# Performance work log

Hardware: AMD Instinct MI355X
Metric: run time of the kernel (lower is better)

Reference implementation:

```python
import jax, jax.numpy as jnp
import numpy as np

DIM = 512
A_HEADS = 8
C_HEADS = 4
DH = 64
EPS = 1e-5


def layer_norm(x, g, b):
    mu = jnp.mean(x, axis=-1, keepdims=True)
    var = jnp.var(x, axis=-1, keepdims=True)
    return (x - mu) * jax.lax.rsqrt(var + EPS) * g + b


def setup_inputs() -> dict:
    key = jax.random.key(0)
    ks = jax.random.split(key, 8)
    inner_a = A_HEADS * DH  # 512
    inner_c = C_HEADS * DH  # 256
    s = 0.02
    return {
        "x": jax.random.normal(ks[0], (4, 192, DIM), dtype=jnp.float32),
        # Attention branch params
        "ln1_g": jnp.ones((DIM,), jnp.float32),
        "ln1_b": jnp.zeros((DIM,), jnp.float32),
        "Wqkv": jax.random.normal(ks[1], (DIM, 3 * inner_a), jnp.float32) * s,
        "Wo": jax.random.normal(ks[2], (inner_a, DIM), jnp.float32) * s,
        "bo": jnp.zeros((DIM,), jnp.float32),
        # Trittention branch params
        "ln2_g": jnp.ones((DIM,), jnp.float32),
        "ln2_b": jnp.zeros((DIM,), jnp.float32),
        "Wabcde": jax.random.normal(ks[3], (DIM, 5 * inner_c), jnp.float32) * s,
        "babcde": jnp.zeros((5 * inner_c,), jnp.float32),
        "Wp": jax.random.normal(ks[4], (inner_c, DIM), jnp.float32) * s,
        "bp": jnp.zeros((DIM,), jnp.float32),
    }


def _attention(x, ln_g, ln_b, Wqkv, Wo, bo):
    B, T, _ = x.shape
    xn = layer_norm(x, ln_g, ln_b)
    qkv = xn @ Wqkv  # [B,T,3*H*D]
    q, k, v = jnp.split(qkv, 3, axis=-1)
    def heads(t):
        return t.reshape(B, T, A_HEADS, DH).transpose(0, 2, 1, 3)  # [B,H,T,D]
    q, k, v = heads(q), heads(k), heads(v)
    scale = DH ** -0.5
    dots = jnp.einsum('bhqd,bhkd->bhqk', q, k) * scale
    attn = jax.nn.softmax(dots, axis=-1)
    out = jnp.einsum('bhqk,bhkd->bhqd', attn, v)
    out = out.transpose(0, 2, 1, 3).reshape(B, T, A_HEADS * DH)
    return out @ Wo + bo


def _trittention(x, ln_g, ln_b, Wabcde, babcde, Wp, bp):
    B, T, _ = x.shape
    xn = layer_norm(x, ln_g, ln_b)
    proj = xn @ Wabcde + babcde  # [B,T,5*H*D]
    a, b_, c, d_, e = jnp.split(proj, 5, axis=-1)
    def heads(t):
        return t.reshape(B, T, C_HEADS, DH)  # [B,T,H,D]
    a, b_, c, d_, e = heads(a), heads(b_), heads(c), heads(d_), heads(e)
    # cubic score: [B,H,S,T,Q]
    score = jnp.einsum('bshd,bthd,bqhd->bhstq', a, b_, c) / DH
    # softmax over joint (s,t) for each query q
    score = score.transpose(0, 1, 4, 2, 3).reshape(B, C_HEADS, T, T * T)
    attn = jax.nn.softmax(score, axis=-1).reshape(B, C_HEADS, T, T, T)
    z = (jnp.einsum('bhqst,bshd->bhqd', attn, d_)
         + jnp.einsum('bhqst,bthd->bhqd', attn, e))
    z = z.transpose(0, 2, 1, 3).reshape(B, T, C_HEADS * DH)
    return z @ Wp + bp


def reference(x, ln1_g, ln1_b, Wqkv, Wo, bo, ln2_g, ln2_b, Wabcde, babcde, Wp, bp):
    return (_attention(x, ln1_g, ln1_b, Wqkv, Wo, bo)
            + _trittention(x, ln2_g, ln2_b, Wabcde, babcde, Wp, bp))
```

## Files before the change

kernel.cpp:

```cpp
#include <hip/hip_runtime.h>
#include <cstdint>


#define B_   4
#define T_   192
#define DIM_ 512
#define AH   8
#define CH   4

typedef unsigned short u16;
typedef unsigned int   u32;
typedef __attribute__((ext_vector_type(8))) short short8;
typedef __attribute__((ext_vector_type(4))) float floatx4;
typedef __attribute__((ext_vector_type(4))) int intx4;
typedef __attribute__((ext_vector_type(2))) float f32x2;
typedef __attribute__((ext_vector_type(8))) _Float16 half8;
typedef __attribute__((ext_vector_type(2))) _Float16 half2v;
typedef __attribute__((ext_vector_type(2))) __fp16 fp16x2;

union Frag  { intx4 i; short8 s; };
union FragH { intx4 i; half8 h; };

__device__ __forceinline__ floatx4 mfma16(Frag a, Frag b, floatx4 c) {
    return __builtin_amdgcn_mfma_f32_16x16x32_bf16(a.s, b.s, c, 0, 0, 0);
}
__device__ __forceinline__ floatx4 mfma16h(FragH a, FragH b, floatx4 c) {
    return __builtin_amdgcn_mfma_f32_16x16x32_f16(a.h, b.h, c, 0, 0, 0);
}

__device__ __forceinline__ float fexp2(float x) {
    return __builtin_amdgcn_exp2f(x);
}

__device__ __forceinline__ float wave_reduce_sum(float v) {
#pragma unroll
    for (int off = 32; off >= 1; off >>= 1)
        v += __shfl_xor(v, off, 64);
    return v;
}

__device__ __forceinline__ u32 pack_rne(float x, float y) {
    u32 ux = __float_as_uint(x);
    u32 uy = __float_as_uint(y);
    ux += 0x7fffu + ((ux >> 16) & 1u);
    uy += 0x7fffu + ((uy >> 16) & 1u);
    return (ux >> 16) | (uy & 0xffff0000u);
}
__device__ __forceinline__ u16 bf16_rne(float x) {
    u32 u = __float_as_uint(x);
    u += 0x7fffu + ((u >> 16) & 1u);
    return (u16)(u >> 16);
}
__device__ __forceinline__ float bf16f(u16 h) { return __uint_as_float(((u32)h) << 16); }

__device__ __forceinline__ u32 pack_f16(float x, float y) {
    union { fp16x2 h; u32 u; } cv;
    cv.h = __builtin_amdgcn_cvt_pkrtz(x, y);
    return cv.u;
}
__device__ __forceinline__ u32 mul_h2(u32 a, u32 b) {
    union { u32 u; half2v h; } ua, ub, uw;
    ua.u = a; ub.u = b;
    uw.h = ua.h * ub.h;
    return uw.u;
}

__device__ __forceinline__ Frag ld_frag8(const u16* p) {
    Frag f;
    uint2 a = *(const uint2*)p;
    uint2 b = *(const uint2*)(p + 4);
    f.i = (intx4){ (int)a.x, (int)a.y, (int)b.x, (int)b.y };
    return f;
}

#define LOG2E 1.44269504088896f

__global__ __launch_bounds__(256) void prep_kernel(
    const float* __restrict__ x,
    const float* __restrict__ g1, const float* __restrict__ b1,
    const float* __restrict__ g2, const float* __restrict__ b2,
    u16* __restrict__ x1h, u16* __restrict__ x2h,
    const float* __restrict__ Wqkv, u16* __restrict__ wqh,
    const float* __restrict__ Wab,  u16* __restrict__ wah,
    const float* __restrict__ Wo,   const float* __restrict__ Wp,
    u16* __restrict__ wofh)
{
    __shared__ union { float t[64][65]; float red[4][2]; } u;
    const int tid = threadIdx.x;
    if (blockIdx.x < 768) {
        int row = blockIdx.x;
        const float2 v = ((const float2*)(x + (size_t)row * DIM_))[tid];
        float s  = v.x + v.y;
        float s2 = v.x * v.x + v.y * v.y;
        s  = wave_reduce_sum(s);
        s2 = wave_reduce_sum(s2);
        int w = tid >> 6;
        if ((tid & 63) == 0) { u.red[w][0] = s; u.red[w][1] = s2; }
        __syncthreads();
        float ts  = u.red[0][0] + u.red[1][0] + u.red[2][0] + u.red[3][0];
        float ts2 = u.red[0][1] + u.red[1][1] + u.red[2][1] + u.red[3][1];
        float mean = ts * (1.0f / DIM_);
        float var  = ts2 * (1.0f / DIM_) - mean * mean;
        float rstd = rsqrtf(var + 1e-5f);
        int c0 = tid * 2;
        float n0 = (v.x - mean) * rstd;
        float n1 = (v.y - mean) * rstd;
        float a0 = n0 * g1[c0] + b1[c0], a1 = n1 * g1[c0 + 1] + b1[c0 + 1];
        float c2 = n0 * g2[c0] + b2[c0], c3 = n1 * g2[c0 + 1] + b2[c0 + 1];
        size_t o = (size_t)row * 256 + tid;
        ((u32*)x1h)[o] = pack_rne(a0, a1);
        ((u32*)x2h)[o] = pack_rne(c2, c3);
        return;
    }
    int id = blockIdx.x - 768;
    const float* W; u16 *H; int K, N, Kout, kofs, tile;
    if (id < 192)      { W = Wqkv; H = wqh;  K = 512; N = 1536; Kout = 512; kofs = 0;   tile = id;       }
    else if (id < 352) { W = Wab;  H = wah;  K = 512; N = 1280; Kout = 512; kofs = 0;   tile = id - 192; }
    else if (id < 416) { W = Wo;   H = wofh; K = 512; N = 512;  Kout = 768; kofs = 0;   tile = id - 352; }
    else               { W = Wp;   H = wofh; K = 256; N = 512;  Kout = 768; kofs = 512; tile = id - 416; }
    int nx = N >> 6;
    int n0 = (tile % nx) * 64, k0 = (tile / nx) * 64;
    int rr = tid >> 4, c4 = (tid & 15) << 2;
#pragma unroll
    for (int p = 0; p < 4; ++p) {
        int row = rr + p * 16;
        float4 v = *(const float4*)(W + (size_t)(k0 + row) * N + n0 + c4);
        u.t[row][c4 + 0] = v.x; u.t[row][c4 + 1] = v.y;
        u.t[row][c4 + 2] = v.z; u.t[row][c4 + 3] = v.w;
    }
    __syncthreads();
#pragma unroll
    for (int p = 0; p < 4; ++p) {
        int n = rr + p * 16;
        u16 hi[4];
#pragma unroll
        for (int c = 0; c < 4; ++c)
            hi[c] = bf16_rne(u.t[c4 + c][n]);
        size_t o = (size_t)(n0 + n) * Kout + kofs + k0 + c4;
        *(uint2*)&H[o] = make_uint2((u32)hi[0] | ((u32)hi[1] << 16), (u32)hi[2] | ((u32)hi[3] << 16));
    }
}

__global__ __launch_bounds__(256) void gemm_dual(
    const u16* __restrict__ x1h, const u16* __restrict__ wqh,
    const u16* __restrict__ x2h, const u16* __restrict__ wah,
    const float* __restrict__ babcde,
    float* __restrict__ qkv, float* __restrict__ proj)
{
    __shared__ u16 As[64][68];
    __shared__ u16 Bs[64][68];
    const int tid = threadIdx.x;
    const int nb = blockIdx.x;
    const u16 *Ah, *BTh; const float* bias; float* C; int N, bn;
    if (nb < 24) { Ah = x1h; BTh = wqh; bias = nullptr; C = qkv;  N = 1536; bn = nb * 64; }
    else         { Ah = x2h; BTh = wah; bias = babcde; C = proj; N = 1280; bn = (nb - 24) * 64; }
    const int K = 512;
    const int bm = blockIdx.y * 64;
    const int lane = tid & 63, wave = tid >> 6;
    const int m16 = lane & 15, quad = lane >> 4;
    const int wm = (wave >> 1) * 32, wn = (wave & 1) * 32;
    const int r = tid >> 2, c16 = (tid & 3) * 16;

    floatx4 acc[2][2];
#pragma unroll
    for (int i = 0; i < 2; ++i)
#pragma unroll
        for (int j = 0; j < 2; ++j) acc[i][j] = (floatx4){0.f, 0.f, 0.f, 0.f};

    for (int k0 = 0; k0 < K; k0 += 64) {
        __syncthreads();
        {
            const u16* pa = Ah + (size_t)(bm + r) * K + k0 + c16;
            uint4 v0 = *(const uint4*)pa, v1 = *(const uint4*)(pa + 8);
            *(uint2*)&As[r][c16 + 0]  = make_uint2(v0.x, v0.y);
            *(uint2*)&As[r][c16 + 4]  = make_uint2(v0.z, v0.w);
            *(uint2*)&As[r][c16 + 8]  = make_uint2(v1.x, v1.y);
            *(uint2*)&As[r][c16 + 12] = make_uint2(v1.z, v1.w);
        }
        {
            const u16* pb = BTh + (size_t)(bn + r) * K + k0 + c16;
            uint4 v0 = *(const uint4*)pb, v1 = *(const uint4*)(pb + 8);
            *(uint2*)&Bs[r][c16 + 0]  = make_uint2(v0.x, v0.y);
            *(uint2*)&Bs[r][c16 + 4]  = make_uint2(v0.z, v0.w);
            *(uint2*)&Bs[r][c16 + 8]  = make_uint2(v1.x, v1.y);
            *(uint2*)&Bs[r][c16 + 12] = make_uint2(v1.z, v1.w);
        }
        __syncthreads();
#pragma unroll
        for (int ks = 0; ks < 2; ++ks) {
            const int ko = ks * 32 + quad * 8;
            Frag a0 = ld_frag8(&As[wm + m16][ko]);
            Frag a1 = ld_frag8(&As[wm + 16 + m16][ko]);
            Frag b0 = ld_frag8(&Bs[wn + m16][ko]);
            Frag b1 = ld_frag8(&Bs[wn + 16 + m16][ko]);
            acc[0][0] = mfma16(a0, b0, acc[0][0]);
            acc[0][1] = mfma16(a0, b1, acc[0][1]);
            acc[1][0] = mfma16(a1, b0, acc[1][0]);
            acc[1][1] = mfma16(a1, b1, acc[1][1]);
        }
    }
#pragma unroll
    for (int i = 0; i < 2; ++i)
#pragma unroll
        for (int rr = 0; rr < 4; ++rr) {
            int m = bm + wm + i * 16 + quad * 4 + rr;
#pragma unroll
            for (int j = 0; j < 2; ++j) {
                int n = bn + wn + j * 16 + m16;
                float v = acc[i][j][rr];
                if (bias) v += bias[n];
                C[(size_t)m * N + n] = v;
            }
        }
}

__global__ __launch_bounds__(256) void gemm_epilogue(
    const u16* __restrict__ aoh, const u16* __restrict__ zh,
    const u16* __restrict__ BTh,
    const float* __restrict__ bo, const float* __restrict__ bp,
    float* __restrict__ C)
{
    __shared__ u16 As[32][68];
    __shared__ u16 Bs[64][68];
    const int tid = threadIdx.x;
    const int bm = blockIdx.y * 32, bn = blockIdx.x * 64;
    const int lane = tid & 63, wave = tid >> 6;
    const int m16 = lane & 15, quad = lane >> 4;
    const int wm = (wave >> 1) * 16, wn = (wave & 1) * 32;
    const int ra = tid >> 3, c8 = (tid & 7) * 8;
    const int rb = tid >> 2, c16 = (tid & 3) * 16;
    const int N = 512, K = 768;

    floatx4 acc[2];
    acc[0] = (floatx4){0.f, 0.f, 0.f, 0.f};
    acc[1] = (floatx4){0.f, 0.f, 0.f, 0.f};

    for (int k0 = 0; k0 < K; k0 += 64) {
        __syncthreads();
        {
            const u16* pah = (k0 < 512)
                ? aoh + (size_t)(bm + ra) * 512 + k0 + c8
                : zh  + (size_t)(bm + ra) * 256 + (k0 - 512) + c8;
            uint4 v = *(const uint4*)pah;
            *(uint2*)&As[ra][c8 + 0] = make_uint2(v.x, v.y);
            *(uint2*)&As[ra][c8 + 4] = make_uint2(v.z, v.w);
        }
        {
            const u16* pb = BTh + (size_t)(bn + rb) * K + k0 + c16;
            uint4 v0 = *(const uint4*)pb, v1 = *(const uint4*)(pb + 8);
            *(uint2*)&Bs[rb][c16 + 0]  = make_uint2(v0.x, v0.y);
            *(uint2*)&Bs[rb][c16 + 4]  = make_uint2(v0.z, v0.w);
            *(uint2*)&Bs[rb][c16 + 8]  = make_uint2(v1.x, v1.y);
            *(uint2*)&Bs[rb][c16 + 12] = make_uint2(v1.z, v1.w);
        }
        __syncthreads();
#pragma unroll
        for (int ks = 0; ks < 2; ++ks) {
            const int ko = ks * 32 + quad * 8;
            Frag ah = ld_frag8(&As[wm + m16][ko]);
            Frag b0 = ld_frag8(&Bs[wn + m16][ko]);
            Frag b1 = ld_frag8(&Bs[wn + 16 + m16][ko]);
            acc[0] = mfma16(ah, b0, acc[0]);
            acc[1] = mfma16(ah, b1, acc[1]);
        }
    }
#pragma unroll
    for (int rr = 0; rr < 4; ++rr) {
        int m = bm + wm + quad * 4 + rr;
#pragma unroll
        for (int j = 0; j < 2; ++j) {
            int n = bn + wn + j * 16 + m16;
            C[(size_t)m * N + n] = acc[j][rr] + bo[n] + bp[n];
        }
    }
}

__global__ __launch_bounds__(256) void attn_mfma(
    const float* __restrict__ qkv, u16* __restrict__ aoh, float* __restrict__ zero_base)
{
    __shared__ union { u16 Ks[192][68]; u16 P[32][196]; } KP;
    __shared__ union { u16 Vt[64][196]; struct { float m[2][16][68]; float r[2][16]; } mg; } VU;
    const int qt = blockIdx.x, h = blockIdx.y, b = blockIdx.z;
    const int tid = threadIdx.x;
    {
        float4* z4 = (float4*)zero_base;
        const float4 z = make_float4(0.f, 0.f, 0.f, 0.f);
        int gid = ((b * AH + h) * 6 + qt) * 256 + tid;
        for (int i = gid; i < 294912; i += 49152) z4[i] = z;
    }
    const int lane = tid & 63, wave = tid >> 6;
    const int m16 = lane & 15, quad = lane >> 4;
    const int qg = wave & 1;
    const int kh = wave >> 1;
    const size_t base = (size_t)(b * T_) * 1536 + h * 64;

    for (int i = tid; i < 192 * 16; i += 256) {
        int row = i >> 4, c4 = (i & 15) << 2;
        float4 kv = *(const float4*)(qkv + base + (size_t)row * 1536 + 512 + c4);
        *(uint2*)&KP.Ks[row][c4] = make_uint2(pack_rne(kv.x, kv.y), pack_rne(kv.z, kv.w));
        float4 vv = *(const float4*)(qkv + base + (size_t)row * 1536 + 1024 + c4);
        VU.Vt[c4 + 0][row] = bf16_rne(vv.x);
        VU.Vt[c4 + 1][row] = bf16_rne(vv.y);
        VU.Vt[c4 + 2][row] = bf16_rne(vv.z);
        VU.Vt[c4 + 3][row] = bf16_rne(vv.w);
    }

    Frag qf0, qf1;
    {
        const float s = 0.125f * LOG2E;
        const float* qp = qkv + base + (size_t)(qt * 32 + qg * 16 + m16) * 1536 + quad * 8;
        float4 u0 = *(const float4*)qp;
        float4 u1 = *(const float4*)(qp + 4);
        float4 u2 = *(const float4*)(qp + 32);
        float4 u3 = *(const float4*)(qp + 36);
        qf0.i = (intx4){ (int)pack_rne(u0.x * s, u0.y * s), (int)pack_rne(u0.z * s, u0.w * s),
                         (int)pack_rne(u1.x * s, u1.y * s), (int)pack_rne(u1.z * s, u1.w * s) };
        qf1.i = (intx4){ (int)pack_rne(u2.x * s, u2.y * s), (int)pack_rne(u2.z * s, u2.w * s),
                         (int)pack_rne(u3.x * s, u3.y * s), (int)pack_rne(u3.z * s, u3.w * s) };
    }
    __syncthreads();

    float ev[6][4];
    float rsum[4] = {0.f, 0.f, 0.f, 0.f};
#pragma unroll
    for (int tt = 0; tt < 6; ++tt) {
        const int krow = kh * 96 + tt * 16 + m16;
        Frag kb0 = ld_frag8(&KP.Ks[krow][quad * 8]);
        Frag kb1 = ld_frag8(&KP.Ks[krow][32 + quad * 8]);
        floatx4 accs = (floatx4){0.f, 0.f, 0.f, 0.f};
        accs = mfma16(qf0, kb0, accs);
        accs = mfma16(qf1, kb1, accs);
#pragma unroll
        for (int rr = 0; rr < 4; ++rr) {
            float e = fexp2(accs[rr]);
            ev[tt][rr] = e;
            rsum[rr] += e;
        }
    }
#pragma unroll
    for (int rr = 0; rr < 4; ++rr) {
        float v = rsum[rr];
        v += __shfl_xor(v, 1, 64);
        v += __shfl_xor(v, 2, 64);
        v += __shfl_xor(v, 4, 64);
        v += __shfl_xor(v, 8, 64);
        rsum[rr] = v;
    }

    __syncthreads();
#pragma unroll
    for (int tt = 0; tt < 6; ++tt)
#pragma unroll
        for (int rr = 0; rr < 4; ++rr)
            KP.P[qg * 16 + quad * 4 + rr][kh * 96 + tt * 16 + m16] = bf16_rne(ev[tt][rr]);

    floatx4 acco[4];
#pragma unroll
    for (int dt = 0; dt < 4; ++dt) acco[dt] = (floatx4){0.f, 0.f, 0.f, 0.f};
#pragma unroll
    for (int ts = 0; ts < 3; ++ts) {
        Frag pf = ld_frag8(&KP.P[qg * 16 + m16][kh * 96 + ts * 32 + quad * 8]);
#pragma unroll
        for (int dt = 0; dt < 4; ++dt) {
            Frag vf = ld_frag8(&VU.Vt[dt * 16 + m16][kh * 96 + ts * 32 + quad * 8]);
            acco[dt] = mfma16(pf, vf, acco[dt]);
        }
    }

    __syncthreads();
    if (kh == 1) {
#pragma unroll
        for (int dt = 0; dt < 4; ++dt)
#pragma unroll
            for (int rr = 0; rr < 4; ++rr)
                VU.mg.m[qg][quad * 4 + rr][dt * 16 + m16] = acco[dt][rr];
        if (m16 == 0) {
#pragma unroll
            for (int rr = 0; rr < 4; ++rr)
                VU.mg.r[qg][quad * 4 + rr] = rsum[rr];
        }
    }
    __syncthreads();
    if (kh == 0) {
        float rinv[4];
#pragma unroll
        for (int rr = 0; rr < 4; ++rr)
            rinv[rr] = 1.0f / (rsum[rr] + VU.mg.r[qg][quad * 4 + rr]);
#pragma unroll
        for (int dt = 0; dt < 4; ++dt)
#pragma unroll
            for (int rr = 0; rr < 4; ++rr) {
                float o = (acco[dt][rr] + VU.mg.m[qg][quad * 4 + rr][dt * 16 + m16]) * rinv[rr];
                size_t idx = (size_t)(b * T_ + qt * 32 + qg * 16 + quad * 4 + rr) * 512
                           + h * 64 + dt * 16 + m16;
                aoh[idx] = bf16_rne(o);
            }
    }
}

__global__ __launch_bounds__(256, 3) void tritt_score_mfma(
    const float* __restrict__ proj, float* __restrict__ rs1, float* __restrict__ rt1)
{
    __shared__ u32 a_lds[48 * 36];
    __shared__ u32 b_lds[48 * 36];
    __shared__ float rs_lds[48][33];
    __shared__ float rt_lds[48][33];

    const int h = blockIdx.y, b = blockIdx.z;
    const int qt = blockIdx.x >> 4;
    const int sc = (blockIdx.x >> 2) & 3;
    const int tc = blockIdx.x & 3;
    const int q0 = qt * 32, s0 = sc * 48, t0 = tc * 48;
    const int tid  = threadIdx.x;
    const int lane = tid & 63, wave = tid >> 6;
    const int m16  = lane & 15, quad = lane >> 4;
    const int bh = b * CH + h;
    const size_t rowbase = (size_t)(b * T_) * 1280 + h * 64;
    const float kA = 0.015625f * LOG2E;

    for (int i = tid; i < 48 * 32; i += 256) {
        int row = i >> 5, cp = i & 31;
        const float2 va = *(const float2*)(proj + rowbase + (size_t)(s0 + row) * 1280 + 0 + cp * 2);
        a_lds[row * 36 + cp] = pack_f16(va.x * kA, va.y * kA);
        const float2 vb = *(const float2*)(proj + rowbase + (size_t)(t0 + row) * 1280 + 256 + cp * 2);
        b_lds[row * 36 + cp] = pack_f16(vb.x, vb.y);
    }

    FragH cf[2][2];
#pragma unroll
    for (int jq = 0; jq < 2; ++jq) {
        const float* cp = proj + rowbase + (size_t)(q0 + jq * 16 + m16) * 1280 + 512 + quad * 8;
        float4 u0 = *(const float4*)(cp);
        float4 u1 = *(const float4*)(cp + 4);
        float4 u2 = *(const float4*)(cp + 32);
        float4 u3 = *(const float4*)(cp + 36);
        cf[jq][0].i = (intx4){ (int)pack_f16(u0.x, u0.y), (int)pack_f16(u0.z, u0.w),
                               (int)pack_f16(u1.x, u1.y), (int)pack_f16(u1.z, u1.w) };
        cf[jq][1].i = (intx4){ (int)pack_f16(u2.x, u2.y), (int)pack_f16(u2.z, u2.w),
                               (int)pack_f16(u3.x, u3.y), (int)pack_f16(u3.z, u3.w) };
    }
    __syncthreads();

    float rt_acc[3][4][2] = {};

    for (int si = 0; si < 12; ++si) {
        const int srow = wave * 12 + si;
        const intx4 av0 = *(const intx4*)(a_lds + srow * 36 + quad * 4);
        const intx4 av1 = *(const intx4*)(a_lds + srow * 36 + 16 + quad * 4);
        float rs_s[2] = {0.f, 0.f};
#pragma unroll
        for (int tt = 0; tt < 3; ++tt) {
            const u32* bp = b_lds + (tt * 16 + m16) * 36;
            intx4 bv0 = *(const intx4*)(bp + quad * 4);
            intx4 bv1 = *(const intx4*)(bp + 16 + quad * 4);
            FragH w0, w1;
#pragma unroll
            for (int j = 0; j < 4; ++j) {
                w0.i[j] = (int)mul_h2((u32)av0[j], (u32)bv0[j]);
                w1.i[j] = (int)mul_h2((u32)av1[j], (u32)bv1[j]);
            }
#pragma unroll
            for (int jq = 0; jq < 2; ++jq) {
                floatx4 acc = (floatx4){0.f, 0.f, 0.f, 0.f};
                acc = mfma16h(w0, cf[jq][0], acc);
                acc = mfma16h(w1, cf[jq][1], acc);
#pragma unroll
                for (int rr = 0; rr < 4; ++rr) {
                    float e = fexp2(acc[rr]);
                    rt_acc[tt][rr][jq] += e;
                    rs_s[jq] += e;
                }
            }
        }
#pragma unroll
        for (int jq = 0; jq < 2; ++jq) {
            float v = rs_s[jq];
            v += __shfl_xor(v, 16, 64);
            v += __shfl_xor(v, 32, 64);
            if (lane < 16) rs_lds[srow][jq * 16 + m16] = v;
        }
    }

    __syncthreads();
    for (int w = 0; w < 4; ++w) {
        if (wave == w) {
#pragma unroll
            for (int tt = 0; tt < 3; ++tt)
#pragma unroll
                for (int rr = 0; rr < 4; ++rr) {
                    int t = tt * 16 + quad * 4 + rr;
#pragma unroll
                    for (int jq = 0; jq < 2; ++jq) {
                        if (w == 0) rt_lds[t][jq * 16 + m16] = rt_acc[tt][rr][jq];
                        else        rt_lds[t][jq * 16 + m16] += rt_acc[tt][rr][jq];
                    }
                }
        }
        __syncthreads();
    }
    for (int i = tid; i < 32 * 48; i += 256) {
        int qq = i / 48, ss = i - qq * 48;
        unsafeAtomicAdd(&rs1[((size_t)bh * T_ + q0 + qq) * T_ + s0 + ss], rs_lds[ss][qq]);
    }
    for (int i = tid; i < 32 * 48; i += 256) {
        int qq = i / 48, t2 = i - qq * 48;
        unsafeAtomicAdd(&rt1[((size_t)bh * T_ + q0 + qq) * T_ + t0 + t2], rt_lds[t2][qq]);
    }
}

__global__ __launch_bounds__(256) void zgemm(
    const float* __restrict__ rs1, const float* __restrict__ rt1,
    const float* __restrict__ proj, u16* __restrict__ zzh)
{
    __shared__ u16 As[2][32][68];
    __shared__ u16 Bs[64][68];
    __shared__ float zred[32][9];
    __shared__ float Zl[32];
    const int mt = blockIdx.x, bh = blockIdx.y;
    const int b = bh >> 2, h = bh & 3;
    const int q0 = mt * 32;
    const int tid = threadIdx.x;
    const int lane = tid & 63, wave = tid >> 6;
    const int m16 = lane & 15, quad = lane >> 4;
    const int wm = (wave >> 1) * 16, wn = (wave & 1) * 32;
    const int ra = tid >> 3, c8 = (tid & 7) * 8;
    const int sl = tid >> 2, d4b = (tid & 3) * 4;

    float zacc = 0.f;
    floatx4 acc[2];
    acc[0] = (floatx4){0.f, 0.f, 0.f, 0.f};
    acc[1] = (floatx4){0.f, 0.f, 0.f, 0.f};

    for (int k0 = 0; k0 < 384; k0 += 64) {
        __syncthreads();
        {
            float g[8];
            if (k0 < 192) {
                const float* p = rs1 + ((size_t)bh * T_ + q0 + ra) * T_ + k0 + c8;
                float4 v0 = *(const float4*)(p);
                float4 v1 = *(const float4*)(p + 4);
                g[0] = v0.x; g[1] = v0.y; g[2] = v0.z; g[3] = v0.w;
                g[4] = v1.x; g[5] = v1.y; g[6] = v1.z; g[7] = v1.w;
                zacc += ((g[0] + g[1]) + (g[2] + g[3])) + ((g[4] + g[5]) + (g[6] + g[7]));
            } else {
                const float* p = rt1 + ((size_t)bh * T_ + q0 + ra) * T_ + (k0 - 192) + c8;
                float4 v0 = *(const float4*)(p);
                float4 v1 = *(const float4*)(p + 4);
                g[0] = v0.x; g[1] = v0.y; g[2] = v0.z; g[3] = v0.w;
                g[4] = v1.x; g[5] = v1.y; g[6] = v1.z; g[7] = v1.w;
            }
#pragma unroll
            for (int i = 0; i < 8; ++i) {
                u16 hi = bf16_rne(g[i]);
                As[0][ra][c8 + i] = hi;
                As[1][ra][c8 + i] = bf16_rne(g[i] - bf16f(hi));
            }
        }
        {
            const int colbase = (k0 < 192 ? 768 : 1024) + h * 64;
            const int s0 = (k0 < 192 ? k0 : k0 - 192);
#pragma unroll
            for (int i = 0; i < 4; ++i) {
                int dd = d4b + i * 16;
                float4 v = *(const float4*)(proj + (size_t)(b * T_ + s0 + sl) * 1280 + colbase + dd);
                Bs[dd + 0][sl] = bf16_rne(v.x);
                Bs[dd + 1][sl] = bf16_rne(v.y);
                Bs[dd + 2][sl] = bf16_rne(v.z);
                Bs[dd + 3][sl] = bf16_rne(v.w);
            }
        }
        __syncthreads();
#pragma unroll
        for (int ks = 0; ks < 2; ++ks) {
            const int ko = ks * 32 + quad * 8;
            Frag gh = ld_frag8(&As[0][wm + m16][ko]);
            Frag gl = ld_frag8(&As[1][wm + m16][ko]);
            Frag d0 = ld_frag8(&Bs[wn + m16][ko]);
            Frag d1 = ld_frag8(&Bs[wn + 16 + m16][ko]);
            acc[0] = mfma16(gh, d0, acc[0]);
            acc[0] = mfma16(gl, d0, acc[0]);
            acc[1] = mfma16(gh, d1, acc[1]);
            acc[1] = mfma16(gl, d1, acc[1]);
        }
    }
    zred[ra][tid & 7] = zacc;
    __syncthreads();
    if (tid < 32) {
        float s = ((zred[tid][0] + zred[tid][1]) + (zred[tid][2] + zred[tid][3]))
                + ((zred[tid][4] + zred[tid][5]) + (zred[tid][6] + zred[tid][7]));
        Zl[tid] = 1.0f / s;
    }
    __syncthreads();
#pragma unroll
    for (int j = 0; j < 2; ++j)
#pragma unroll
        for (int rr = 0; rr < 4; ++rr) {
            int m = wm + quad * 4 + rr;
            int d = wn + j * 16 + m16;
            float zv = acc[j][rr] * Zl[m];
            size_t idx = (size_t)(b * T_ + q0 + m) * 256 + h * 64 + d;
            zzh[idx] = bf16_rne(zv);
        }
}

extern "C" void kernel_launch(void* const* d_in, const int* in_sizes, int n_in,
                              void* d_out, int out_size, void* d_ws, size_t ws_size,
                              hipStream_t stream)
{
    const float* x      = (const float*)d_in[0];
    const float* ln1_g  = (const float*)d_in[1];
    const float* ln1_b  = (const float*)d_in[2];
    const float* Wqkv   = (const float*)d_in[3];
    const float* Wo     = (const float*)d_in[4];
    const float* bo     = (const float*)d_in[5];
    const float* ln2_g  = (const float*)d_in[6];
    const float* ln2_b  = (const float*)d_in[7];
    const float* Wabcde = (const float*)d_in[8];
    const float* babcde = (const float*)d_in[9];
    const float* Wp     = (const float*)d_in[10];
    const float* bp     = (const float*)d_in[11];
    float* out = (float*)d_out;

    float* ws   = (float*)d_ws;
    float* proj = ws;
    u16* wofh   = (u16*)(proj + 983040);
    u16* aoh    = (u16*)(ws + 1376256);
    u16* zh     = (u16*)(ws + 1769472);
    float* qkv  = ws + 1966080;
    float* rs1  = ws + 1966080 + 1179648;
    float* rt1  = rs1 + 589824;
    u16* x1h = (u16*)rs1;
    u16* x2h = x1h + 393216;
    u16* wqh = (u16*)(rt1 + 589824);
    u16* wah = wqh + 786432;

    prep_kernel<<<1216, 256, 0, stream>>>(x, ln1_g, ln1_b, ln2_g, ln2_b,
                                          x1h, x2h,
                                          Wqkv, wqh, Wabcde, wah,
                                          Wo, Wp, wofh);
    gemm_dual<<<dim3(44, 12), 256, 0, stream>>>(x1h, wqh, x2h, wah,
                                                babcde, qkv, proj);
    attn_mfma<<<dim3(6, AH, B_), 256, 0, stream>>>(qkv, aoh, rs1);
    tritt_score_mfma<<<dim3(96, CH, B_), 256, 0, stream>>>(proj, rs1, rt1);
    zgemm<<<dim3(6, 16), 256, 0, stream>>>(rs1, rt1, proj, zh);
    gemm_epilogue<<<dim3(8, 24), 256, 0, stream>>>(aoh, zh, wofh, bo, bp, out);
}
```

Measured before the change: 158.2 us.

## Fuse attention and trittention score kernels into one launch, move zeroing to prep

Merges the attention kernel and the trittention score kernel into a single launch. Block index selects the branch: 96 attention blocks and 1536 trittention blocks share one LDS union. Attention now uses 64-query blocks with a two-pass loop over key halves, replacing the cross-wave merge. Zeroing of the rs1/rt1 accumulation buffers moves into prep_kernel, and the workspace is relaid so they no longer alias the bf16 activation buffers. This removes one launch and the serialization between the two kernels. In exchange the attention blocks have fewer, larger tiles and may become a tail on the combined grid.

```diff
diff --git a/kernel.cpp b/kernel.cpp
--- a/kernel.cpp
+++ b/kernel.cpp
@@ -83,10 +83,14 @@
     const float* __restrict__ Wqkv, u16* __restrict__ wqh,
     const float* __restrict__ Wab,  u16* __restrict__ wah,
     const float* __restrict__ Wo,   const float* __restrict__ Wp,
-    u16* __restrict__ wofh)
+    u16* __restrict__ wofh, float* __restrict__ zero_base)
 {
     __shared__ union { float t[64][65]; float red[4][2]; } u;
     const int tid = threadIdx.x;
+    {
+        int gid = blockIdx.x * 256 + tid;
+        if (gid < 294912) ((float4*)zero_base)[gid] = make_float4(0.f, 0.f, 0.f, 0.f);
+    }
     if (blockIdx.x < 768) {
         int row = blockIdx.x;
         const float2 v = ((const float2*)(x + (size_t)row * DIM_))[tid];
@@ -275,145 +279,129 @@
     }
 }
 
-__global__ __launch_bounds__(256) void attn_mfma(
-    const float* __restrict__ qkv, u16* __restrict__ aoh, float* __restrict__ zero_base)
+__global__ __launch_bounds__(256, 3) void attn_tritt(
+    const float* __restrict__ qkv, const float* __restrict__ proj,
+    u16* __restrict__ aoh, float* __restrict__ rs1, float* __restrict__ rt1)
 {
-    __shared__ union { u16 Ks[192][68]; u16 P[32][196]; } KP;
-    __shared__ union { u16 Vt[64][196]; struct { float m[2][16][68]; float r[2][16]; } mg; } VU;
-    const int qt = blockIdx.x, h = blockIdx.y, b = blockIdx.z;
+    __shared__ union {
+        struct {
+            union { u16 Ks[96][68]; u16 P[64][100]; } kp;
+            u16 Vt[64][100];
+        } at;
+        struct {
+            u32 a_lds[48 * 36];
+            u32 b_lds[48 * 36];
+            float rs_lds[48][33];
+            float rt_lds[48][33];
+        } tr;
+    } S;
     const int tid = threadIdx.x;
-    {
-        float4* z4 = (float4*)zero_base;
-        const float4 z = make_float4(0.f, 0.f, 0.f, 0.f);
-        int gid = ((b * AH + h) * 6 + qt) * 256 + tid;
-        for (int i = gid; i < 294912; i += 49152) z4[i] = z;
-    }
     const int lane = tid & 63, wave = tid >> 6;
     const int m16 = lane & 15, quad = lane >> 4;
-    const int qg = wave & 1;
-    const int kh = wave >> 1;
-    const size_t base = (size_t)(b * T_) * 1536 + h * 64;
-
-    for (int i = tid; i < 192 * 16; i += 256) {
-        int row = i >> 4, c4 = (i & 15) << 2;
-        float4 kv = *(const float4*)(qkv + base + (size_t)row * 1536 + 512 + c4);
-        *(uint2*)&KP.Ks[row][c4] = make_uint2(pack_rne(kv.x, kv.y), pack_rne(kv.z, kv.w));
-        float4 vv = *(const float4*)(qkv + base + (size_t)row * 1536 + 1024 + c4);
-        VU.Vt[c4 + 0][row] = bf16_rne(vv.x);
-        VU.Vt[c4 + 1][row] = bf16_rne(vv.y);
-        VU.Vt[c4 + 2][row] = bf16_rne(vv.z);
-        VU.Vt[c4 + 3][row] = bf16_rne(vv.w);
-    }
-
-    Frag qf0, qf1;
-    {
-        const float s = 0.125f * LOG2E;
-        const float* qp = qkv + base + (size_t)(qt * 32 + qg * 16 + m16) * 1536 + quad * 8;
-        float4 u0 = *(const float4*)qp;
-        float4 u1 = *(const float4*)(qp + 4);
-        float4 u2 = *(const float4*)(qp + 32);
-        float4 u3 = *(const float4*)(qp + 36);
-        qf0.i = (intx4){ (int)pack_rne(u0.x * s, u0.y * s), (int)pack_rne(u0.z * s, u0.w * s),
-                         (int)pack_rne(u1.x * s, u1.y * s), (int)pack_rne(u1.z * s, u1.w * s) };
-        qf1.i = (intx4){ (int)pack_rne(u2.x * s, u2.y * s), (int)pack_rne(u2.z * s, u2.w * s),
-                         (int)pack_rne(u3.x * s, u3.y * s), (int)pack_rne(u3.z * s, u3.w * s) };
-    }
-    __syncthreads();
-
-    float ev[6][4];
-    float rsum[4] = {0.f, 0.f, 0.f, 0.f};
-#pragma unroll
-    for (int tt = 0; tt < 6; ++tt) {
-        const int krow = kh * 96 + tt * 16 + m16;
-        Frag kb0 = ld_frag8(&KP.Ks[krow][quad * 8]);
-        Frag kb1 = ld_frag8(&KP.Ks[krow][32 + quad * 8]);
-        floatx4 accs = (floatx4){0.f, 0.f, 0.f, 0.f};
-        accs = mfma16(qf0, kb0, accs);
-        accs = mfma16(qf1, kb1, accs);
+
+    if (blockIdx.x < 96) {
+        const int ab = blockIdx.x;
+        const int b = ab / 24, rem = ab % 24;
+        const int h = rem / 3, qt3 = rem % 3;
+        const int qg = wave;
+        const size_t base = (size_t)(b * T_) * 1536 + h * 64;
+
+        Frag qf0, qf1;
+        {
+            const float s = 0.125f * LOG2E;
+            const float* qp = qkv + base + (size_t)(qt3 * 64 + qg * 16 + m16) * 1536 + quad * 8;
+            float4 u0 = *(const float4*)qp;
+            float4 u1 = *(const float4*)(qp + 4);
+            float4 u2 = *(const float4*)(qp + 32);
+            float4 u3 = *(const float4*)(qp + 36);
+            qf0.i = (intx4){ (int)pack_rne(u0.x * s, u0.y * s), (int)pack_rne(u0.z * s, u0.w * s),
+                             (int)pack_rne(u1.x * s, u1.y * s), (int)pack_rne(u1.z * s, u1.w * s) };
+            qf1.i = (intx4){ (int)pack_rne(u2.x * s, u2.y * s), (int)pack_rne(u2.z * s, u2.w * s),
+                             (int)pack_rne(u3.x * s, u3.y * s), (int)pack_rne(u3.z * s, u3.w * s) };
+        }
+
+        float rsum[4] = {0.f, 0.f, 0.f, 0.f};
+        floatx4 acco[4];
+#pragma unroll
+        for (int dt = 0; dt < 4; ++dt) acco[dt] = (floatx4){0.f, 0.f, 0.f, 0.f};
+
+        for (int p = 0; p < 2; ++p) {
+            if (p) __syncthreads();
+            for (int i = tid; i < 96 * 16; i += 256) {
+                int row = i >> 4, c4 = (i & 15) << 2;
+                const float* kp = qkv + base + (size_t)(p * 96 + row) * 1536 + 512 + c4;
+                float4 kv = *(const float4*)kp;
+                *(uint2*)&S.at.kp.Ks[row][c4] = make_uint2(pack_rne(kv.x, kv.y), pack_rne(kv.z, kv.w));
+                float4 vv = *(const float4*)(qkv + base + (size_t)(p * 96 + row) * 1536 + 1024 + c4);
+                S.at.Vt[c4 + 0][row] = bf16_rne(vv.x);
+                S.at.Vt[c4 + 1][row] = bf16_rne(vv.y);
+                S.at.Vt[c4 + 2][row] = bf16_rne(vv.z);
+                S.at.Vt[c4 + 3][row] = bf16_rne(vv.w);
+            }
+            __syncthreads();
+
+            float ev[6][4];
+#pragma unroll
+            for (int tt = 0; tt < 6; ++tt) {
+                Frag kb0 = ld_frag8(&S.at.kp.Ks[tt * 16 + m16][quad * 8]);
+                Frag kb1 = ld_frag8(&S.at.kp.Ks[tt * 16 + m16][32 + quad * 8]);
+                floatx4 accs = (floatx4){0.f, 0.f, 0.f, 0.f};
+                accs = mfma16(qf0, kb0, accs);
+                accs = mfma16(qf1, kb1, accs);
+#pragma unroll
+                for (int rr = 0; rr < 4; ++rr) {
+                    float e = fexp2(accs[rr]);
+                    ev[tt][rr] = e;
+                    rsum[rr] += e;
+                }
+            }
+            __syncthreads();
+#pragma unroll
+            for (int tt = 0; tt < 6; ++tt)
+#pragma unroll
+                for (int rr = 0; rr < 4; ++rr)
+                    S.at.kp.P[qg * 16 + quad * 4 + rr][tt * 16 + m16] = bf16_rne(ev[tt][rr]);
+#pragma unroll
+            for (int ts = 0; ts < 3; ++ts) {
+                Frag pf = ld_frag8(&S.at.kp.P[qg * 16 + m16][ts * 32 + quad * 8]);
+#pragma unroll
+                for (int dt = 0; dt < 4; ++dt) {
+                    Frag vf = ld_frag8(&S.at.Vt[dt * 16 + m16][ts * 32 + quad * 8]);
+                    acco[dt] = mfma16(pf, vf, acco[dt]);
+                }
+            }
+        }
+
+        float rinv[4];
 #pragma unroll
         for (int rr = 0; rr < 4; ++rr) {
-            float e = fexp2(accs[rr]);
-            ev[tt][rr] = e;
-            rsum[rr] += e;
-        }
-    }
-#pragma unroll
-    for (int rr = 0; rr < 4; ++rr) {
-        float v = rsum[rr];
-        v += __shfl_xor(v, 1, 64);
-        v += __shfl_xor(v, 2, 64);
-        v += __shfl_xor(v, 4, 64);
-        v += __shfl_xor(v, 8, 64);
-        rsum[rr] = v;
-    }
-
-    __syncthreads();
-#pragma unroll
-    for (int tt = 0; tt < 6; ++tt)
-#pragma unroll
-        for (int rr = 0; rr < 4; ++rr)
-            KP.P[qg * 16 + quad * 4 + rr][kh * 96 + tt * 16 + m16] = bf16_rne(ev[tt][rr]);
-
-    floatx4 acco[4];
-#pragma unroll
-    for (int dt = 0; dt < 4; ++dt) acco[dt] = (floatx4){0.f, 0.f, 0.f, 0.f};
-#pragma unroll
-    for (int ts = 0; ts < 3; ++ts) {
-        Frag pf = ld_frag8(&KP.P[qg * 16 + m16][kh * 96 + ts * 32 + quad * 8]);
-#pragma unroll
-        for (int dt = 0; dt < 4; ++dt) {
-            Frag vf = ld_frag8(&VU.Vt[dt * 16 + m16][kh * 96 + ts * 32 + quad * 8]);
-            acco[dt] = mfma16(pf, vf, acco[dt]);
-        }
-    }
-
-    __syncthreads();
-    if (kh == 1) {
+            float v = rsum[rr];
+            v += __shfl_xor(v, 1, 64);
+            v += __shfl_xor(v, 2, 64);
+            v += __shfl_xor(v, 4, 64);
+            v += __shfl_xor(v, 8, 64);
+            rinv[rr] = 1.0f / v;
+        }
 #pragma unroll
         for (int dt = 0; dt < 4; ++dt)
 #pragma unroll
-            for (int rr = 0; rr < 4; ++rr)
-                VU.mg.m[qg][quad * 4 + rr][dt * 16 + m16] = acco[dt][rr];
-        if (m16 == 0) {
-#pragma unroll
-            for (int rr = 0; rr < 4; ++rr)
-                VU.mg.r[qg][quad * 4 + rr] = rsum[rr];
-        }
-    }
-    __syncthreads();
-    if (kh == 0) {
-        float rinv[4];
-#pragma unroll
-        for (int rr = 0; rr < 4; ++rr)
-            rinv[rr] = 1.0f / (rsum[rr] + VU.mg.r[qg][quad * 4 + rr]);
-#pragma unroll
-        for (int dt = 0; dt < 4; ++dt)
-#pragma unroll
             for (int rr = 0; rr < 4; ++rr) {
-                float o = (acco[dt][rr] + VU.mg.m[qg][quad * 4 + rr][dt * 16 + m16]) * rinv[rr];
-                size_t idx = (size_t)(b * T_ + qt * 32 + qg * 16 + quad * 4 + rr) * 512
+                float o = acco[dt][rr] * rinv[rr];
+                size_t idx = (size_t)(b * T_ + qt3 * 64 + qg * 16 + quad * 4 + rr) * 512
                            + h * 64 + dt * 16 + m16;
                 aoh[idx] = bf16_rne(o);
             }
-    }
-}
-
-__global__ __launch_bounds__(256, 3) void tritt_score_mfma(
-    const float* __restrict__ proj, float* __restrict__ rs1, float* __restrict__ rt1)
-{
-    __shared__ u32 a_lds[48 * 36];
-    __shared__ u32 b_lds[48 * 36];
-    __shared__ float rs_lds[48][33];
-    __shared__ float rt_lds[48][33];
-
-    const int h = blockIdx.y, b = blockIdx.z;
-    const int qt = blockIdx.x >> 4;
-    const int sc = (blockIdx.x >> 2) & 3;
-    const int tc = blockIdx.x & 3;
+        return;
+    }
+
+    const int t2 = blockIdx.x - 96;
+    const int xx = t2 % 96;
+    const int h = (t2 / 96) % CH;
+    const int b = t2 / (96 * CH);
+    const int qt = xx >> 4;
+    const int sc = (xx >> 2) & 3;
+    const int tc = xx & 3;
     const int q0 = qt * 32, s0 = sc * 48, t0 = tc * 48;
-    const int tid  = threadIdx.x;
-    const int lane = tid & 63, wave = tid >> 6;
-    const int m16  = lane & 15, quad = lane >> 4;
     const int bh = b * CH + h;
     const size_t rowbase = (size_t)(b * T_) * 1280 + h * 64;
     const float kA = 0.015625f * LOG2E;
@@ -421,9 +409,9 @@
     for (int i = tid; i < 48 * 32; i += 256) {
         int row = i >> 5, cp = i & 31;
         const float2 va = *(const float2*)(proj + rowbase + (size_t)(s0 + row) * 1280 + 0 + cp * 2);
-        a_lds[row * 36 + cp] = pack_f16(va.x * kA, va.y * kA);
+        S.tr.a_lds[row * 36 + cp] = pack_f16(va.x * kA, va.y * kA);
         const float2 vb = *(const float2*)(proj + rowbase + (size_t)(t0 + row) * 1280 + 256 + cp * 2);
-        b_lds[row * 36 + cp] = pack_f16(vb.x, vb.y);
+        S.tr.b_lds[row * 36 + cp] = pack_f16(vb.x, vb.y);
     }
 
     FragH cf[2][2];
@@ -445,12 +433,12 @@
 
     for (int si = 0; si < 12; ++si) {
         const int srow = wave * 12 + si;
-        const intx4 av0 = *(const intx4*)(a_lds + srow * 36 + quad * 4);
-        const intx4 av1 = *(const intx4*)(a_lds + srow * 36 + 16 + quad * 4);
+        const intx4 av0 = *(const intx4*)(S.tr.a_lds + srow * 36 + quad * 4);
+        const intx4 av1 = *(const intx4*)(S.tr.a_lds + srow * 36 + 16 + quad * 4);
         float rs_s[2] = {0.f, 0.f};
 #pragma unroll
         for (int tt = 0; tt < 3; ++tt) {
-            const u32* bp = b_lds + (tt * 16 + m16) * 36;
+            const u32* bp = S.tr.b_lds + (tt * 16 + m16) * 36;
             intx4 bv0 = *(const intx4*)(bp + quad * 4);
             intx4 bv1 = *(const intx4*)(bp + 16 + quad * 4);
             FragH w0, w1;
@@ -477,7 +465,7 @@
             float v = rs_s[jq];
             v += __shfl_xor(v, 16, 64);
             v += __shfl_xor(v, 32, 64);
-            if (lane < 16) rs_lds[srow][jq * 16 + m16] = v;
+            if (lane < 16) S.tr.rs_lds[srow][jq * 16 + m16] = v;
         }
     }
 
@@ -491,8 +479,8 @@
                     int t = tt * 16 + quad * 4 + rr;
 #pragma unroll
                     for (int jq = 0; jq < 2; ++jq) {
-                        if (w == 0) rt_lds[t][jq * 16 + m16] = rt_acc[tt][rr][jq];
-                        else        rt_lds[t][jq * 16 + m16] += rt_acc[tt][rr][jq];
+                        if (w == 0) S.tr.rt_lds[t][jq * 16 + m16] = rt_acc[tt][rr][jq];
+                        else        S.tr.rt_lds[t][jq * 16 + m16] += rt_acc[tt][rr][jq];
                     }
                 }
         }
@@ -500,11 +488,11 @@
     }
     for (int i = tid; i < 32 * 48; i += 256) {
         int qq = i / 48, ss = i - qq * 48;
-        unsafeAtomicAdd(&rs1[((size_t)bh * T_ + q0 + qq) * T_ + s0 + ss], rs_lds[ss][qq]);
+        unsafeAtomicAdd(&rs1[((size_t)bh * T_ + q0 + qq) * T_ + s0 + ss], S.tr.rs_lds[ss][qq]);
     }
     for (int i = tid; i < 32 * 48; i += 256) {
-        int qq = i / 48, t2 = i - qq * 48;
-        unsafeAtomicAdd(&rt1[((size_t)bh * T_ + q0 + qq) * T_ + t0 + t2], rt_lds[t2][qq]);
+        int qq = i / 48, t3 = i - qq * 48;
+        unsafeAtomicAdd(&rt1[((size_t)bh * T_ + q0 + qq) * T_ + t0 + t3], S.tr.rt_lds[t3][qq]);
     }
 }
 
@@ -623,25 +611,24 @@
 
     float* ws   = (float*)d_ws;
     float* proj = ws;
-    u16* wofh   = (u16*)(proj + 983040);
-    u16* aoh    = (u16*)(ws + 1376256);
-    u16* zh     = (u16*)(ws + 1769472);
-    float* qkv  = ws + 1966080;
-    float* rs1  = ws + 1966080 + 1179648;
-    float* rt1  = rs1 + 589824;
-    u16* x1h = (u16*)rs1;
-    u16* x2h = x1h + 393216;
-    u16* wqh = (u16*)(rt1 + 589824);
-    u16* wah = wqh + 786432;
+    u16* wofh   = (u16*)(ws + 983040);
+    u16* aoh    = (u16*)(ws + 1179648);
+    u16* zh     = (u16*)(ws + 1376256);
+    float* qkv  = ws + 1474560;
+    u16* x1h    = (u16*)(ws + 2654208);
+    u16* x2h    = (u16*)(ws + 2850816);
+    u16* wqh    = (u16*)(ws + 3047424);
+    u16* wah    = (u16*)(ws + 3440640);
+    float* rs1  = ws + 3768320;
+    float* rt1  = ws + 4358144;
 
     prep_kernel<<<1216, 256, 0, stream>>>(x, ln1_g, ln1_b, ln2_g, ln2_b,
                                           x1h, x2h,
                                           Wqkv, wqh, Wabcde, wah,
-                                          Wo, Wp, wofh);
+                                          Wo, Wp, wofh, rs1);
     gemm_dual<<<dim3(44, 12), 256, 0, stream>>>(x1h, wqh, x2h, wah,
                                                 babcde, qkv, proj);
-    attn_mfma<<<dim3(6, AH, B_), 256, 0, stream>>>(qkv, aoh, rs1);
-    tritt_score_mfma<<<dim3(96, CH, B_), 256, 0, stream>>>(proj, rs1, rt1);
+    attn_tritt<<<96 + 1536, 256, 0, stream>>>(qkv, proj, aoh, rs1, rt1);
     zgemm<<<dim3(6, 16), 256, 0, stream>>>(rs1, rt1, proj, zh);
     gemm_epilogue<<<dim3(8, 24), 256, 0, stream>>>(aoh, zh, wofh, bo, bp, out);
 }
```

Result: faster. 148.4 us (-6.2%).
